# Performance work log

Measured on AMD Instinct MI355X. Metric: run time of the kernel, lower is better.

## Reference

```python
import jax, jax.numpy as jnp
import numpy as np

N, E, G = 16000, 256000, 64
H, NR, L = 128, 96, 2
CUTOFF = 6.0
EPS = 1e-10

def _ln(x, eps=1e-5):
    m = jnp.mean(x, -1, keepdims=True)
    v = jnp.mean((x - m) ** 2, -1, keepdims=True)
    return (x - m) * jax.lax.rsqrt(v + eps)

def _mlp2(x, w1, b1, w2, b2):
    return jax.nn.silu(x @ w1 + b1) @ w2 + b2

def _xav(key, shape):
    s = (2.0 / (shape[-2] + shape[-1])) ** 0.5
    return jax.random.normal(key, shape, jnp.float32) * s

def setup_inputs():
    key = jax.random.key(0)
    ks = iter(jax.random.split(key, 64))
    pos = jax.random.normal(next(ks), (N, 3), jnp.float32) * 2.0
    z = jax.random.randint(next(ks), (N,), 1, 95)
    batch = jnp.sort(jax.random.randint(next(ks), (N,), 0, G))
    src = jax.random.randint(next(ks), (E,), 0, N)
    off = jax.random.randint(next(ks), (E,), 1, N)
    dst = (src + off) % N  # no self loops -> dist > 0
    edge_index = jnp.stack([src, dst]).astype(jnp.int32)
    H3 = 3 * H
    return dict(
        pos=pos,
        z_emb_w=jax.random.normal(next(ks), (95, H), jnp.float32),
        ne_emb_w=jax.random.normal(next(ks), (95, H), jnp.float32),
        rl_w1=_xav(next(ks), (NR, H)), rl_b1=jnp.zeros((H,), jnp.float32),
        rl_w2=_xav(next(ks), (H, H)), rl_b2=jnp.zeros((H,), jnp.float32),
        sv_w=_xav(next(ks), (H, H)), sv_b=jnp.zeros((H,), jnp.float32),
        lin_w1=_xav(next(ks), (3, H // 4)), lin_b1=jnp.zeros((H // 4,), jnp.float32),
        lin_w2=_xav(next(ks), (H // 4, 1)), lin_b2=jnp.zeros((1,), jnp.float32),
        mp_ln_g=jnp.ones((L, H), jnp.float32), mp_ln_b=jnp.zeros((L, H), jnp.float32),
        mp_xw1=_xav(next(ks), (L, H, H)), mp_xb1=jnp.zeros((L, H), jnp.float32),
        mp_xw2=_xav(next(ks), (L, H, H3)), mp_xb2=jnp.zeros((L, H3), jnp.float32),
        mp_rw=_xav(next(ks), (L, NR, H3)), mp_rb=jnp.zeros((L, H3), jnp.float32),
        mp_dw1=_xav(next(ks), (L, H3 + NR, H3)), mp_db1=jnp.zeros((L, H3), jnp.float32),
        mp_dw2=_xav(next(ks), (L, H3, H3)), mp_db2=jnp.zeros((L, H3), jnp.float32),
        ft_vw=_xav(next(ks), (L, H, 2 * H)),
        ft_xw1=_xav(next(ks), (L, 2 * H, H)), ft_xb1=jnp.zeros((L, H), jnp.float32),
        ft_xw2=_xav(next(ks), (L, H, H3)), ft_xb2=jnp.zeros((L, H3), jnp.float32),
        last_w=_xav(next(ks), (H, 1)), last_b=jnp.zeros((1,), jnp.float32),
        z=z, edge_index=edge_index, batch=batch,
    )

def _forward(pos, z_emb_w, ne_emb_w, rl_w1, rl_b1, rl_w2, rl_b2, sv_w, sv_b,
             lin_w1, lin_b1, lin_w2, lin_b2, mp_ln_g, mp_ln_b, mp_xw1, mp_xb1,
             mp_xw2, mp_xb2, mp_rw, mp_rb, mp_dw1, mp_db1, mp_dw2, mp_db2,
             ft_vw, ft_xw1, ft_xb1, ft_xw2, ft_xb2, last_w, last_b,
             z, edge_index, batch):
    inv_sqrt3 = 1.0 / (3.0 ** 0.5)
    inv_sqrt_h = 1.0 / (H ** 0.5)
    inv_sqrt2 = 1.0 / (2.0 ** 0.5)
    src, dst = edge_index[0], edge_index[1]  # gather from src, scatter-add to dst
    edge_vec = pos[src] - pos[dst]                         # (E,3)
    dist = jnp.sqrt(jnp.sum(edge_vec ** 2, -1))            # (E,)
    # rbf_emb buffers
    start = jnp.exp(jnp.float32(-CUTOFF))
    means = jnp.linspace(start, 1.0, NR)
    betas = (2.0 / NR * (1.0 - start)) ** (-2.0)
    d = dist[:, None]
    rbounds = 0.5 * (jnp.cos(dist * jnp.pi / CUTOFF) + 1.0) * (dist < CUTOFF).astype(dist.dtype)
    rbf = rbounds[:, None] * jnp.exp(-betas * (jnp.exp(-d) - means) ** 2)   # (E,NR)
    rh = rbounds[:, None] * _mlp2(rbf, rl_w1, rl_b1, rl_w2, rl_b2)          # (E,H) radial_hidden
    # embeddings + NeighborEmb (gather-scale-scatter)
    s = _ln(z_emb_w[z])
    sn = _ln(ne_emb_w[z])
    s = s + jax.ops.segment_sum(rh * sn[src], dst, num_segments=N)
    vec = jnp.zeros((N, 3, H), pos.dtype)
    # edge-wise equivariant frame
    edge_diff = edge_vec / d
    edge_cross = jnp.cross(pos[src], pos[dst])
    edge_cross = edge_cross / (jnp.linalg.norm(edge_cross, axis=-1, keepdims=True) + EPS)
    edge_vertical = jnp.cross(edge_diff, edge_cross)
    edge_frame = jnp.stack([edge_diff, edge_cross, edge_vertical], -1)      # (E,3,3)
    # S_vector
    s1 = jax.nn.silu(_ln(s @ sv_w + sv_b))
    msgv = (rh[:, None, :] * edge_diff[:, :, None]) * s1[src][:, None, :]   # (E,3,H)
    S_ij = jax.ops.segment_sum(msgv, dst, num_segments=N)                   # (N,3,H)

    def _scalarize(Sg):
        sc = jnp.einsum('eck,ech->ekh', edge_frame, Sg)    # (E,3,H)
        sc = sc.at[:, 1, :].set(jnp.abs(sc[:, 1, :]))
        p = jnp.transpose(sc, (0, 2, 1))                   # (E,H,3)
        out = _mlp2(p, lin_w1, lin_b1, lin_w2, lin_b2) + p[:, :, 0:1]
        return out[..., 0]                                 # (E,H)

    scalar3 = _scalarize(S_ij[src])
    scalar4 = _scalarize(S_ij[dst])
    edge_weight = jnp.concatenate([scalar3, scalar4], -1) * rbounds[:, None]
    edge_weight = jnp.concatenate([edge_weight, rh, rbf], -1)  # (E, 3H+NR)

    for l in range(L):
        # EquiMessagePassing
        xh = _mlp2(mp_ln_g[l] * _ln(s) + mp_ln_b[l], mp_xw1[l], mp_xb1[l], mp_xw2[l], mp_xb2[l])  # (N,3H)
        rbfh = (rbf @ mp_rw[l] + mp_rb[l]) * _mlp2(edge_weight, mp_dw1[l], mp_db1[l], mp_dw2[l], mp_db2[l])
        m = xh[src] * rbfh                                  # (E,3H)
        mx, m2, m3 = jnp.split(m, 3, -1)
        m2 = m2 * inv_sqrt3
        mvec = (vec[src] * m2[:, None, :] + m3[:, None, :] * edge_diff[:, :, None]) * inv_sqrt_h
        s = (s + jax.ops.segment_sum(mx, dst, num_segments=N)) * inv_sqrt2
        vec = vec + jax.ops.segment_sum(mvec, dst, num_segments=N)
        # FTE (node_frame unused by FTE in the original code)
        vp = jnp.einsum('nch,hk->nck', vec, ft_vw[l])       # (N,3,2H)
        v1, v2 = jnp.split(vp, 2, -1)
        scalar = jnp.sqrt(jnp.sum(v1 ** 2, 1) + 1e-10)      # (N,H)
        vec_dot = jnp.sum(v1 * v2, 1) * inv_sqrt_h
        xvh = _mlp2(jnp.concatenate([s, scalar], -1), ft_xw1[l], ft_xb1[l], ft_xw2[l], ft_xb2[l])
        x1, x2, x3 = jnp.split(xvh, 3, -1)
        s = s + (x1 + x2 + vec_dot) * inv_sqrt2
        vec = vec + x3[:, None, :] * v2

    out = s @ last_w + last_b                               # (N,1)
    return jax.ops.segment_sum(out, batch, num_segments=G)  # (G,1) sum readout

def reference(pos, z_emb_w, ne_emb_w, rl_w1, rl_b1, rl_w2, rl_b2, sv_w, sv_b,
              lin_w1, lin_b1, lin_w2, lin_b2, mp_ln_g, mp_ln_b, mp_xw1, mp_xb1,
              mp_xw2, mp_xb2, mp_rw, mp_rb, mp_dw1, mp_db1, mp_dw2, mp_db2,
              ft_vw, ft_xw1, ft_xb1, ft_xw2, ft_xb2, last_w, last_b,
              z, edge_index, batch):
    return _forward(pos, z_emb_w, ne_emb_w, rl_w1, rl_b1, rl_w2, rl_b2, sv_w, sv_b,
                    lin_w1, lin_b1, lin_w2, lin_b2, mp_ln_g, mp_ln_b, mp_xw1, mp_xb1,
                    mp_xw2, mp_xb2, mp_rw, mp_rb, mp_dw1, mp_db1, mp_dw2, mp_db2,
                    ft_vw, ft_xw1, ft_xb1, ft_xw2, ft_xb2, last_w, last_b,
                    z, edge_index, batch)
```

## Files before the change

kernel.cpp:

```cpp
#include <hip/hip_runtime.h>
#include <math.h>

#define NN 16000
#define NE 256000
#define NG 64
#define HD 128
#define NRAD 96
#define H3 384
#define KD 480

typedef unsigned short u16;
typedef short short8 __attribute__((ext_vector_type(8)));
typedef float f32x4 __attribute__((ext_vector_type(4)));

__device__ __forceinline__ float siluf(float x){ return x / (1.0f + expf(-x)); }

__device__ __forceinline__ float wsum(float v){
#pragma unroll
    for (int o = 32; o > 0; o >>= 1) v += __shfl_xor(v, o, 64);
    return v;
}

__device__ __forceinline__ u16 f2bh(float f){
    unsigned int u = __float_as_uint(f);
    unsigned int r = u + 0x7FFFu + ((u >> 16) & 1u);
    return (u16)(r >> 16);
}
__device__ __forceinline__ float bh2f(u16 h){
    return __uint_as_float((unsigned int)h << 16);
}
__device__ __forceinline__ short8 ld8(const u16* p){ return *(const short8*)p; }

__device__ __forceinline__ void split4(float4 v, uint2& ph, uint2& pl){
    unsigned ux = __float_as_uint(v.x), uy = __float_as_uint(v.y);
    unsigned uz = __float_as_uint(v.z), uw = __float_as_uint(v.w);
    ph.x = __builtin_amdgcn_perm(uy, ux, 0x07060302u);
    ph.y = __builtin_amdgcn_perm(uw, uz, 0x07060302u);
    float lx = v.x - __uint_as_float(ux & 0xFFFF0000u);
    float ly = v.y - __uint_as_float(uy & 0xFFFF0000u);
    float lz = v.z - __uint_as_float(uz & 0xFFFF0000u);
    float lw = v.w - __uint_as_float(uw & 0xFFFF0000u);
    pl.x = __builtin_amdgcn_perm(__float_as_uint(ly), __float_as_uint(lx), 0x07060302u);
    pl.y = __builtin_amdgcn_perm(__float_as_uint(lw), __float_as_uint(lz), 0x07060302u);
}

__global__ void k_fill(float* __restrict__ p, float v, int n){
    int i = blockIdx.x * blockDim.x + threadIdx.x;
    if (i < n) p[i] = v;
}

__global__ void k_wsplit(const float* __restrict__ src, u16* __restrict__ dh, int K, int N){
    int i = blockIdx.x * 256 + threadIdx.x;
    if (i >= K * N) return;
    int n = i / K, k = i - n * K;
    dh[i] = f2bh(src[(size_t)k * N + n]);
}

__global__ void k_node_embed(const float* __restrict__ zw, const float* __restrict__ nw,
                             const int* __restrict__ z, float* __restrict__ s, float* __restrict__ sn){
    int n = blockIdx.x, t = threadIdx.x;
    int zi = z[n];
    const float* a = zw + (size_t)zi * HD;
    const float* b = nw + (size_t)zi * HD;
    float a0 = a[t], a1 = a[t + 64];
    float m  = wsum(a0 + a1) * (1.f / HD);
    float va = wsum((a0 - m)*(a0 - m) + (a1 - m)*(a1 - m)) * (1.f / HD);
    float r  = rsqrtf(va + 1e-5f);
    s[(size_t)n*HD + t]      = (a0 - m) * r;
    s[(size_t)n*HD + 64 + t] = (a1 - m) * r;
    float b0 = b[t], b1 = b[t + 64];
    m  = wsum(b0 + b1) * (1.f / HD);
    va = wsum((b0 - m)*(b0 - m) + (b1 - m)*(b1 - m)) * (1.f / HD);
    r  = rsqrtf(va + 1e-5f);
    sn[(size_t)n*HD + t]      = (b0 - m) * r;
    sn[(size_t)n*HD + 64 + t] = (b1 - m) * r;
}

__global__ void k_ln_silu(const float* __restrict__ x, float* __restrict__ out){
    int n = blockIdx.x, t = threadIdx.x;
    float a0 = x[(size_t)n*HD + t], a1 = x[(size_t)n*HD + 64 + t];
    float m  = wsum(a0 + a1) * (1.f / HD);
    float va = wsum((a0 - m)*(a0 - m) + (a1 - m)*(a1 - m)) * (1.f / HD);
    float r  = rsqrtf(va + 1e-5f);
    out[(size_t)n*HD + t]      = siluf((a0 - m) * r);
    out[(size_t)n*HD + 64 + t] = siluf((a1 - m) * r);
}

__global__ void k_ln_aff(const float* __restrict__ x, const float* __restrict__ g,
                         const float* __restrict__ b, float* __restrict__ out){
    int n = blockIdx.x, t = threadIdx.x;
    float a0 = x[(size_t)n*HD + t], a1 = x[(size_t)n*HD + 64 + t];
    float m  = wsum(a0 + a1) * (1.f / HD);
    float va = wsum((a0 - m)*(a0 - m) + (a1 - m)*(a1 - m)) * (1.f / HD);
    float r  = rsqrtf(va + 1e-5f);
    out[(size_t)n*HD + t]      = g[t]      * ((a0 - m) * r) + b[t];
    out[(size_t)n*HD + 64 + t] = g[64 + t] * ((a1 - m) * r) + b[64 + t];
}

__global__ void k_edge_geom(const float* __restrict__ pos, const int* __restrict__ ei,
                            float* __restrict__ dist, float* __restrict__ rbnd,
                            float* __restrict__ frame){
    int e = blockIdx.x * blockDim.x + threadIdx.x;
    if (e >= NE) return;
    int si = ei[e], di = ei[NE + e];
    float sx = pos[si*3], sy = pos[si*3+1], sz = pos[si*3+2];
    float dx = pos[di*3], dy = pos[di*3+1], dz = pos[di*3+2];
    float vx = sx - dx, vy = sy - dy, vz = sz - dz;
    float dd = sqrtf(vx*vx + vy*vy + vz*vz);
    dist[e] = dd;
    float rb = (dd < 6.0f) ? 0.5f * (cosf(dd * 0.5235987755982988f) + 1.0f) : 0.0f;
    rbnd[e] = rb;
    float inv = 1.0f / dd;
    float ux = vx*inv, uy = vy*inv, uz = vz*inv;
    float cx = sy*dz - sz*dy, cy = sz*dx - sx*dz, cz = sx*dy - sy*dx;
    float cn = sqrtf(cx*cx + cy*cy + cz*cz) + 1e-10f;
    cx /= cn; cy /= cn; cz /= cn;
    float wx = uy*cz - uz*cy, wy = uz*cx - ux*cz, wz = ux*cy - uy*cx;
    frame[(0*3+0)*NE + e] = ux; frame[(1*3+0)*NE + e] = uy; frame[(2*3+0)*NE + e] = uz;
    frame[(0*3+1)*NE + e] = cx; frame[(1*3+1)*NE + e] = cy; frame[(2*3+1)*NE + e] = cz;
    frame[(0*3+2)*NE + e] = wx; frame[(1*3+2)*NE + e] = wy; frame[(2*3+2)*NE + e] = wz;
}

__global__ void k_rbf(const float* __restrict__ dist, const float* __restrict__ rbnd,
                      float* __restrict__ base, int e0, int ec){
    int idx = blockIdx.x * 256 + threadIdx.x;
    int e = idx / NRAD;
    if (e >= ec) return;
    int k = idx - e * NRAD;
    int eg = e0 + e;
    float start = expf(-6.0f);
    float mean  = start + (1.0f - start) * ((float)k / 95.0f);
    float c     = (2.0f / 96.0f) * (1.0f - start);
    float betas = 1.0f / (c * c);
    float t = expf(-dist[eg]) - mean;
    base[(size_t)e * KD + k] = rbnd[eg] * expf(-betas * t * t);
}

__global__ __launch_bounds__(256)
void mgemm(const float* __restrict__ A, int lda,
           const u16* __restrict__ Bhg, int K,
           const float* __restrict__ bias, int act,
           float* __restrict__ C, int ldc,
           int M, int Nn,
           const float* __restrict__ row_scale,
           const float* __restrict__ mulC, int ldm){
    __shared__ u16 Ah[128*40], Al[128*40];
    __shared__ u16 Bh[64*40];
    int tid = threadIdx.x;
    int w = tid >> 6, l = tid & 63;
    int row0 = blockIdx.x * 128, col0 = blockIdx.y * 64;
    f32x4 acc[2][4] = {};
    const int r16 = l & 15, kb = (l >> 4) * 8;

    for (int k0 = 0; k0 < K; k0 += 32){
        if (k0) __syncthreads();
#pragma unroll
        for (int i = 0; i < 4; i++){
            int f = tid + i * 256;
            int r = f >> 3, kq = (f & 7) * 4;
            const float4 v = *(const float4*)(A + (size_t)(row0 + r) * lda + k0 + kq);
            uint2 ph, pl;
            split4(v, ph, pl);
            *(uint2*)&Ah[r*40 + kq] = ph;
            *(uint2*)&Al[r*40 + kq] = pl;
        }
        {
            int bn = tid >> 2, kq = (tid & 3) * 8;
            const size_t gb = (size_t)(col0 + bn) * K + k0 + kq;
            *(short8*)&Bh[bn*40 + kq] = ld8(Bhg + gb);
        }
        __syncthreads();
        short8 ah0 = *(const short8*)&Ah[(w*32      + r16)*40 + kb];
        short8 ah1 = *(const short8*)&Ah[(w*32 + 16 + r16)*40 + kb];
        short8 al0 = *(const short8*)&Al[(w*32      + r16)*40 + kb];
        short8 al1 = *(const short8*)&Al[(w*32 + 16 + r16)*40 + kb];
#pragma unroll
        for (int nf = 0; nf < 4; nf++){
            short8 bhv = *(const short8*)&Bh[(nf*16 + r16)*40 + kb];
            acc[0][nf] = __builtin_amdgcn_mfma_f32_16x16x32_bf16(ah0, bhv, acc[0][nf], 0, 0, 0);
            acc[0][nf] = __builtin_amdgcn_mfma_f32_16x16x32_bf16(al0, bhv, acc[0][nf], 0, 0, 0);
            acc[1][nf] = __builtin_amdgcn_mfma_f32_16x16x32_bf16(ah1, bhv, acc[1][nf], 0, 0, 0);
            acc[1][nf] = __builtin_amdgcn_mfma_f32_16x16x32_bf16(al1, bhv, acc[1][nf], 0, 0, 0);
        }
    }
    int rq = (l >> 4) * 4;
#pragma unroll
    for (int mf = 0; mf < 2; mf++){
#pragma unroll
        for (int nf = 0; nf < 4; nf++){
            int n = col0 + nf*16 + r16;
            float bz = bias ? bias[n] : 0.0f;
#pragma unroll
            for (int reg = 0; reg < 4; reg++){
                int m = row0 + w*32 + mf*16 + rq + reg;
                float v = acc[mf][nf][reg] + bz;
                if (act) v = siluf(v);
                if (row_scale) v *= row_scale[m];
                if (mulC) v *= mulC[(size_t)m * ldm + n];
                C[(size_t)m * ldc + n] = v;
            }
        }
    }
}

__global__ __launch_bounds__(256)
void dw2s(const float* __restrict__ hb,
          const float* __restrict__ ewrbf,
          const u16* __restrict__ B1h,
          const u16* __restrict__ B2h,
          const float* __restrict__ rb, const float* __restrict__ db2,
          const float* __restrict__ xh, const float* __restrict__ vec,
          const float* __restrict__ frame, const int* __restrict__ ei,
          float* __restrict__ s, float* __restrict__ vec_acc, int e0){
    __shared__ u16 Ah[128*40], Al[128*40];
    __shared__ u16 Bh[64*40];
    int tid = threadIdx.x;
    int w = tid >> 6, l = tid & 63;
    int row0 = blockIdx.x * 128, col0 = blockIdx.y * 64;
    const int r16 = l & 15, kb = (l >> 4) * 8;
    f32x4 acc1[2][4] = {}, acc2[2][4] = {};

    for (int k0 = 0; k0 < 96; k0 += 32){
        if (k0) __syncthreads();
#pragma unroll
        for (int i = 0; i < 4; i++){
            int f = tid + i * 256;
            int r = f >> 3, kq = (f & 7) * 4;
            const float4 v = *(const float4*)(ewrbf + (size_t)(row0 + r) * KD + k0 + kq);
            uint2 ph, pl;
            split4(v, ph, pl);
            *(uint2*)&Ah[r*40 + kq] = ph;
            *(uint2*)&Al[r*40 + kq] = pl;
        }
        {
            int bn = tid >> 2, kq = (tid & 3) * 8;
            const size_t gb = (size_t)(col0 + bn) * 96 + k0 + kq;
            *(short8*)&Bh[bn*40 + kq] = ld8(B2h + gb);
        }
        __syncthreads();
        short8 ah0 = *(const short8*)&Ah[(w*32      + r16)*40 + kb];
        short8 ah1 = *(const short8*)&Ah[(w*32 + 16 + r16)*40 + kb];
        short8 al0 = *(const short8*)&Al[(w*32      + r16)*40 + kb];
        short8 al1 = *(const short8*)&Al[(w*32 + 16 + r16)*40 + kb];
#pragma unroll
        for (int nf = 0; nf < 4; nf++){
            short8 bhv = *(const short8*)&Bh[(nf*16 + r16)*40 + kb];
            acc2[0][nf] = __builtin_amdgcn_mfma_f32_16x16x32_bf16(ah0, bhv, acc2[0][nf], 0, 0, 0);
            acc2[0][nf] = __builtin_amdgcn_mfma_f32_16x16x32_bf16(al0, bhv, acc2[0][nf], 0, 0, 0);
            acc2[1][nf] = __builtin_amdgcn_mfma_f32_16x16x32_bf16(ah1, bhv, acc2[1][nf], 0, 0, 0);
            acc2[1][nf] = __builtin_amdgcn_mfma_f32_16x16x32_bf16(al1, bhv, acc2[1][nf], 0, 0, 0);
        }
    }
    for (int k0 = 0; k0 < H3; k0 += 32){
        __syncthreads();
#pragma unroll
        for (int i = 0; i < 4; i++){
            int f = tid + i * 256;
            int r = f >> 3, kq = (f & 7) * 4;
            const float4 v = *(const float4*)(hb + (size_t)(row0 + r) * H3 + k0 + kq);
            uint2 ph, pl;
            split4(v, ph, pl);
            *(uint2*)&Ah[r*40 + kq] = ph;
            *(uint2*)&Al[r*40 + kq] = pl;
        }
        {
            int bn = tid >> 2, kq = (tid & 3) * 8;
            const size_t gb = (size_t)(col0 + bn) * H3 + k0 + kq;
            *(short8*)&Bh[bn*40 + kq] = ld8(B1h + gb);
        }
        __syncthreads();
        short8 ah0 = *(const short8*)&Ah[(w*32      + r16)*40 + kb];
        short8 ah1 = *(const short8*)&Ah[(w*32 + 16 + r16)*40 + kb];
        short8 al0 = *(const short8*)&Al[(w*32      + r16)*40 + kb];
        short8 al1 = *(const short8*)&Al[(w*32 + 16 + r16)*40 + kb];
#pragma unroll
        for (int nf = 0; nf < 4; nf++){
            short8 bhv = *(const short8*)&Bh[(nf*16 + r16)*40 + kb];
            acc1[0][nf] = __builtin_amdgcn_mfma_f32_16x16x32_bf16(ah0, bhv, acc1[0][nf], 0, 0, 0);
            acc1[0][nf] = __builtin_amdgcn_mfma_f32_16x16x32_bf16(al0, bhv, acc1[0][nf], 0, 0, 0);
            acc1[1][nf] = __builtin_amdgcn_mfma_f32_16x16x32_bf16(ah1, bhv, acc1[1][nf], 0, 0, 0);
            acc1[1][nf] = __builtin_amdgcn_mfma_f32_16x16x32_bf16(al1, bhv, acc1[1][nf], 0, 0, 0);
        }
    }
    int rq = (l >> 4) * 4;
    int br = col0 >> 7;
    int ho = col0 & 127;
#pragma unroll
    for (int mf = 0; mf < 2; mf++){
#pragma unroll
        for (int reg = 0; reg < 4; reg++){
            int m  = row0 + w*32 + mf*16 + rq + reg;
            int eg = e0 + m;
            int si = ei[eg], di = ei[NE + eg];
            float df0 = 0.f, df1 = 0.f, df2 = 0.f;
            if (br == 2){
                df0 = frame[0*NE + eg];
                df1 = frame[3*NE + eg];
                df2 = frame[6*NE + eg];
            }
#pragma unroll
            for (int nf = 0; nf < 4; nf++){
                int n = col0 + nf*16 + r16;
                int h = ho + nf*16 + r16;
                float v  = (acc2[mf][nf][reg] + rb[n]) * (acc1[mf][nf][reg] + db2[n]);
                float xv = xh[(size_t)si * H3 + n];
                if (br == 0){
                    atomicAdd(&s[(size_t)di * HD + h], xv * v);
                } else if (br == 1){
                    float m2 = xv * v * 0.5773502691896258f;
                    size_t sb = (size_t)si * H3, db = (size_t)di * H3;
#pragma unroll
                    for (int c = 0; c < 3; c++)
                        atomicAdd(&vec_acc[db + c*HD + h],
                                  vec[sb + c*HD + h] * m2 * 0.08838834764831845f);
                } else {
                    float m3 = xv * v * 0.08838834764831845f;
                    size_t db = (size_t)di * H3;
                    atomicAdd(&vec_acc[db + 0*HD + h], m3 * df0);
                    atomicAdd(&vec_acc[db + 1*HD + h], m3 * df1);
                    atomicAdd(&vec_acc[db + 2*HD + h], m3 * df2);
                }
            }
        }
    }
}

struct WT { u16* h; };

static void gemm(hipStream_t st, const float* A, int lda, WT B,
                 const float* bias, float* C, int ldc, size_t M, int K, int Nn,
                 int act, const float* rs, const float* mul, int ldm){
    dim3 g((unsigned)(M / 128), (unsigned)(Nn / 64)), b(256);
    mgemm<<<g, b, 0, st>>>(A, lda, B.h, K, bias, act, C, ldc, (int)M, Nn, rs, mul, ldm);
}

__global__ void k_scatter_s(const float* __restrict__ rh, const float* __restrict__ sn,
                            const int* __restrict__ ei, float* __restrict__ s, int e0, int ec,
                            long long stride){
    int idx = blockIdx.x * 256 + threadIdx.x;
    int e = idx >> 7, h = idx & 127;
    if (e >= ec) return;
    int eg = e0 + e;
    int si = ei[eg], di = ei[NE + eg];
    atomicAdd(&s[(size_t)di * HD + h], rh[(size_t)e * stride + h] * sn[(size_t)si * HD + h]);
}

__global__ void k_scatter_msgv(const float* __restrict__ rh, const float* __restrict__ s1,
                               const float* __restrict__ frame, const int* __restrict__ ei,
                               float* __restrict__ S_ij, int e0, int ec){
    int idx = blockIdx.x * 256 + threadIdx.x;
    int e = idx >> 7, h = idx & 127;
    if (e >= ec) return;
    int eg = e0 + e;
    int si = ei[eg], di = ei[NE + eg];
    float mv = rh[(size_t)e * KD + h] * s1[(size_t)si * HD + h];
    size_t db = (size_t)di * H3;
#pragma unroll
    for (int c = 0; c < 3; c++){
        float df = frame[(c*3 + 0) * NE + eg];
        atomicAdd(&S_ij[db + c * HD + h], mv * df);
    }
}

__global__ void k_scalarize(const float* __restrict__ S_ij, const float* __restrict__ frame,
                            const float* __restrict__ rbnd, const int* __restrict__ ei,
                            const float* __restrict__ w1, const float* __restrict__ b1,
                            const float* __restrict__ w2, const float* __restrict__ b2v,
                            float* __restrict__ base, int e0){
    int e = blockIdx.x, h = threadIdx.x;
    int eg = e0 + e;
    int si = ei[eg], di = ei[NE + eg];
    float fr[9];
#pragma unroll
    for (int i = 0; i < 9; i++) fr[i] = frame[i * NE + eg];
    float rb = rbnd[eg];
    float b2 = b2v[0];
#pragma unroll
    for (int g = 0; g < 2; g++){
        int node = g ? di : si;
        float S0 = S_ij[(size_t)node * H3 + h];
        float S1 = S_ij[(size_t)node * H3 + 128 + h];
        float S2 = S_ij[(size_t)node * H3 + 256 + h];
        float p0 = fr[0]*S0 + fr[3]*S1 + fr[6]*S2;
        float p1 = fabsf(fr[1]*S0 + fr[4]*S1 + fr[7]*S2);
        float p2 = fr[2]*S0 + fr[5]*S1 + fr[8]*S2;
        float o = b2 + p0;
#pragma unroll
        for (int j = 0; j < 32; j++){
            float hh = siluf(p0 * w1[j] + p1 * w1[32 + j] + p2 * w1[64 + j] + b1[j]);
            o += hh * w2[j];
        }
        base[(size_t)e * KD + g * 128 + h] = o * rb;
    }
}

__global__ void k_scale_vecadd(float* __restrict__ s, float* __restrict__ vec,
                               const float* __restrict__ vec_acc){
    int i = blockIdx.x * 256 + threadIdx.x;
    vec[i] += vec_acc[i];
    int n = i / H3, r = i - n * H3;
    if (r < HD) s[(size_t)n * HD + r] *= 0.7071067811865476f;
}

__global__ void k_vfeat(const float* __restrict__ vp, const float* __restrict__ s,
                        float* __restrict__ t256, float* __restrict__ vdot){
    int idx = blockIdx.x * 256 + threadIdx.x;
    int n = idx >> 7, h = idx & 127;
    float a = 0.f, b = 0.f;
#pragma unroll
    for (int c = 0; c < 3; c++){
        float v1 = vp[(size_t)(n*3 + c) * 256 + h];
        float v2 = vp[(size_t)(n*3 + c) * 256 + 128 + h];
        a += v1 * v1;
        b += v1 * v2;
    }
    t256[(size_t)n * 256 + 128 + h] = sqrtf(a + 1e-10f);
    vdot[idx] = b * 0.08838834764831845f;
    t256[(size_t)n * 256 + h] = s[idx];
}

__global__ void k_upd(float* __restrict__ s, float* __restrict__ vec,
                      const float* __restrict__ xvh, const float* __restrict__ vp,
                      const float* __restrict__ vdot){
    int idx = blockIdx.x * 256 + threadIdx.x;
    int n = idx / H3;
    int r = idx - n * H3;
    int c = r >> 7, h = r & 127;
    vec[idx] += xvh[(size_t)n * H3 + 256 + h] * vp[(size_t)(n*3 + c) * 256 + 128 + h];
    if (c == 0){
        size_t si = (size_t)n * HD + h;
        s[si] += (xvh[(size_t)n * H3 + h] + xvh[(size_t)n * H3 + 128 + h]
                  + vdot[si]) * 0.7071067811865476f;
    }
}

__global__ void k_final(const float* __restrict__ s, const float* __restrict__ lw,
                        const float* __restrict__ lb, const int* __restrict__ batch,
                        float* __restrict__ out){
    int n = blockIdx.x, t = threadIdx.x;
    float v = s[(size_t)n * HD + t] * lw[t] + s[(size_t)n * HD + 64 + t] * lw[64 + t];
    v = wsum(v);
    if (t == 0) atomicAdd(&out[batch[n]], v + lb[0]);
}

extern "C" void kernel_launch(void* const* d_in, const int* in_sizes, int n_in,
                              void* d_out, int out_size, void* d_ws, size_t ws_size,
                              hipStream_t stream){
    const float* pos      = (const float*)d_in[0];
    const float* z_emb_w  = (const float*)d_in[1];
    const float* ne_emb_w = (const float*)d_in[2];
    const float* rl_w1    = (const float*)d_in[3];
    const float* rl_b1    = (const float*)d_in[4];
    const float* rl_w2    = (const float*)d_in[5];
    const float* rl_b2    = (const float*)d_in[6];
    const float* sv_w     = (const float*)d_in[7];
    const float* sv_b     = (const float*)d_in[8];
    const float* lin_w1   = (const float*)d_in[9];
    const float* lin_b1   = (const float*)d_in[10];
    const float* lin_w2   = (const float*)d_in[11];
    const float* lin_b2   = (const float*)d_in[12];
    const float* mp_ln_g  = (const float*)d_in[13];
    const float* mp_ln_b  = (const float*)d_in[14];
    const float* mp_xw1   = (const float*)d_in[15];
    const float* mp_xb1   = (const float*)d_in[16];
    const float* mp_xw2   = (const float*)d_in[17];
    const float* mp_xb2   = (const float*)d_in[18];
    const float* mp_rw    = (const float*)d_in[19];
    const float* mp_rb    = (const float*)d_in[20];
    const float* mp_dw1   = (const float*)d_in[21];
    const float* mp_db1   = (const float*)d_in[22];
    const float* mp_dw2   = (const float*)d_in[23];
    const float* mp_db2   = (const float*)d_in[24];
    const float* ft_vw    = (const float*)d_in[25];
    const float* ft_xw1   = (const float*)d_in[26];
    const float* ft_xb1   = (const float*)d_in[27];
    const float* ft_xw2   = (const float*)d_in[28];
    const float* ft_xb2   = (const float*)d_in[29];
    const float* last_w   = (const float*)d_in[30];
    const float* last_b   = (const float*)d_in[31];
    const int*   z        = (const int*)d_in[32];
    const int*   ei       = (const int*)d_in[33];
    const int*   batch    = (const int*)d_in[34];
    float* out = (float*)d_out;
    (void)in_sizes; (void)n_in; (void)out_size;

    float* ws = (float*)d_ws;
    size_t off = 0;
    auto alloc = [&](size_t nf){ float* p = ws + off; off += (nf + 63) & ~(size_t)63; return p; };

    float* s       = alloc((size_t)NN * HD);
    float* sn      = alloc((size_t)NN * HD);
    float* s1      = alloc((size_t)NN * HD);
    float* tA      = alloc((size_t)NN * HD);
    float* vdot    = alloc((size_t)NN * HD);
    float* vec     = alloc((size_t)NN * H3);
    float* vec_acc = alloc((size_t)NN * H3);
    float* S_ij    = alloc((size_t)NN * H3);
    float* xh      = alloc((size_t)NN * H3);
    float* vp      = alloc((size_t)NN * 3 * 256);
    float* dist    = alloc((size_t)NE);
    float* rbnd    = alloc((size_t)NE);
    float* frame   = alloc((size_t)NE * 9);
    float* t256    = sn;

    const size_t WELEMS = 45056 + 2 * 548864;
    u16* wcur = (u16*)alloc((WELEMS + 1) / 2);
    auto wsplit = [&](const float* src, int K, int N)->WT{
        WT r; r.h = wcur; wcur += (size_t)K * N;
        k_wsplit<<<(unsigned)(((size_t)K * N + 255) / 256), 256, 0, stream>>>(src, r.h, K, N);
        return r;
    };
    WT W_rl1 = wsplit(rl_w1, NRAD, HD);
    WT W_rl2 = wsplit(rl_w2, HD, HD);
    WT W_sv  = wsplit(sv_w, HD, HD);
    WT W_xw1[2], W_xw2[2], W_rw[2], W_dw1[2], W_dw2[2], W_vw[2], W_fx1[2], W_fx2[2];
    for (int l = 0; l < 2; l++){
        W_xw1[l] = wsplit(mp_xw1 + (size_t)l * HD * HD, HD, HD);
        W_xw2[l] = wsplit(mp_xw2 + (size_t)l * HD * H3, HD, H3);
        W_rw[l]  = wsplit(mp_rw  + (size_t)l * NRAD * H3, NRAD, H3);
        W_dw1[l] = wsplit(mp_dw1 + (size_t)l * KD * H3, KD, H3);
        W_dw2[l] = wsplit(mp_dw2 + (size_t)l * H3 * H3, H3, H3);
        W_vw[l]  = wsplit(ft_vw  + (size_t)l * HD * 256, HD, 256);
        W_fx1[l] = wsplit(ft_xw1 + (size_t)l * 256 * HD, 256, HD);
        W_fx2[l] = wsplit(ft_xw2 + (size_t)l * HD * H3, HD, H3);
    }

    size_t availF = ws_size / sizeof(float);
    size_t rem = (availF > off + 1024) ? (availF - off - 1024) : 0;
    const size_t EWF = (size_t)NE * KD;
    bool persist;
    size_t CE;
    float* ew  = nullptr;
    float* ewc = nullptr;
    if (rem >= EWF + 128 * 384 + 256){
        persist = true;
        ew = alloc(EWF);
        rem = availF - off - 1024;
        size_t ce = rem / (size_t)H3;
        CE = ce & ~(size_t)127;
        if (CE < 128) CE = 128;
        if (CE > NE) CE = NE;
    } else {
        persist = false;
        size_t ce = rem / ((size_t)KD + (size_t)H3);
        CE = ce & ~(size_t)127;
        if (CE < 128) CE = 128;
        if (CE > NE) CE = NE;
    }
    if (CE > 32768) CE = 32768;
    if (!persist) ewc = alloc(CE * KD);
    size_t hbufF = CE * (size_t)H3;
    bool full_layer = false;
    if (persist){
        size_t remNow = (availF > off + 1024) ? (availF - off - 1024) : 0;
        const size_t FULLH = (size_t)NE * H3;
        if (remNow >= FULLH){ hbufF = FULLH; full_layer = true; }
    }
    float* hbuf = alloc(hbufF);

    auto build_rh = [&](size_t e0, size_t ec, float* base){
        k_rbf<<<(unsigned)((ec * NRAD) / 256), 256, 0, stream>>>(dist, rbnd, base + 384, (int)e0, (int)ec);
        gemm(stream, base + 384, KD, W_rl1, rl_b1, hbuf, HD, ec, NRAD, HD, 1, nullptr, nullptr, 0);
        gemm(stream, hbuf, HD, W_rl2, rl_b2, base + 256, KD, ec, HD, HD, 0, rbnd + e0, nullptr, 0);
    };

    k_fill<<<1, 64, 0, stream>>>(out, 0.f, NG);
    k_node_embed<<<NN, 64, 0, stream>>>(z_emb_w, ne_emb_w, z, s, sn);
    k_edge_geom<<<NE / 256, 256, 0, stream>>>(pos, ei, dist, rbnd, frame);

    if (persist){
        k_rbf<<<(unsigned)(((size_t)NE * NRAD) / 256), 256, 0, stream>>>(dist, rbnd, ew + 384, 0, NE);
        if (full_layer){
            gemm(stream, ew + 384, KD, W_rl1, rl_b1, hbuf, HD, NE, NRAD, HD, 1, nullptr, nullptr, 0);
            gemm(stream, hbuf, HD, W_rl2, rl_b2, ew + 256, KD, NE, HD, HD, 0, rbnd, nullptr, 0);
        } else {
            for (size_t e0 = 0; e0 < NE; e0 += CE){
                size_t ec = (NE - e0 < CE) ? (NE - e0) : CE;
                float* base = ew + e0 * KD;
                gemm(stream, base + 384, KD, W_rl1, rl_b1, hbuf, HD, ec, NRAD, HD, 1, nullptr, nullptr, 0);
                gemm(stream, hbuf, HD, W_rl2, rl_b2, base + 256, KD, ec, HD, HD, 0, rbnd + e0, nullptr, 0);
            }
        }
        k_scatter_s<<<(unsigned)(((size_t)NE * HD) / 256), 256, 0, stream>>>(ew + 256, sn, ei, s, 0, NE, KD);
    } else {
        for (size_t e0 = 0; e0 < NE; e0 += CE){
            size_t ec = (NE - e0 < CE) ? (NE - e0) : CE;
            build_rh(e0, ec, ewc);
            k_scatter_s<<<(unsigned)((ec * HD) / 256), 256, 0, stream>>>(ewc + 256, sn, ei, s, (int)e0, (int)ec, KD);
        }
    }

    gemm(stream, s, HD, W_sv, sv_b, tA, HD, NN, HD, HD, 0, nullptr, nullptr, 0);
    k_ln_silu<<<NN, 64, 0, stream>>>(tA, s1);

    k_fill<<<(NN * H3) / 256, 256, 0, stream>>>(S_ij, 0.f, NN * H3);
    if (persist){
        k_scatter_msgv<<<(unsigned)(((size_t)NE * HD) / 256), 256, 0, stream>>>(ew + 256, s1, frame, ei, S_ij, 0, NE);
        k_scalarize<<<NE, 128, 0, stream>>>(S_ij, frame, rbnd, ei, lin_w1, lin_b1, lin_w2, lin_b2, ew, 0);
    } else {
        for (size_t e0 = 0; e0 < NE; e0 += CE){
            size_t ec = (NE - e0 < CE) ? (NE - e0) : CE;
            build_rh(e0, ec, ewc);
            k_scatter_msgv<<<(unsigned)((ec * HD) / 256), 256, 0, stream>>>(ewc + 256, s1, frame, ei, S_ij, (int)e0, (int)ec);
        }
    }

    k_fill<<<(NN * H3) / 256, 256, 0, stream>>>(vec, 0.f, NN * H3);

    for (int l = 0; l < 2; l++){
        k_ln_aff<<<NN, 64, 0, stream>>>(s, mp_ln_g + l * HD, mp_ln_b + l * HD, tA);
        gemm(stream, tA, HD, W_xw1[l], mp_xb1 + l * HD, vdot, HD, NN, HD, HD, 1, nullptr, nullptr, 0);
        gemm(stream, vdot, HD, W_xw2[l], mp_xb2 + l * H3, xh, H3, NN, HD, H3, 0, nullptr, nullptr, 0);

        k_fill<<<(NN * H3) / 256, 256, 0, stream>>>(vec_acc, 0.f, NN * H3);

        if (full_layer){
            gemm(stream, ew, KD, W_dw1[l], mp_db1 + l * H3, hbuf, H3, NE, KD, H3, 1, nullptr, nullptr, 0);
            dim3 g((unsigned)(NE / 128), 6);
            dw2s<<<g, 256, 0, stream>>>(hbuf, ew + 384,
                                        W_dw2[l].h, W_rw[l].h,
                                        mp_rb + l * H3, mp_db2 + l * H3,
                                        xh, vec, frame, ei, s, vec_acc, 0);
        } else {
            for (size_t e0 = 0; e0 < NE; e0 += CE){
                size_t ec = (NE - e0 < CE) ? (NE - e0) : CE;
                float* base = persist ? (ew + e0 * KD) : ewc;
                if (!persist){
                    build_rh(e0, ec, base);
                    k_scalarize<<<(unsigned)ec, 128, 0, stream>>>(S_ij, frame, rbnd, ei, lin_w1, lin_b1, lin_w2, lin_b2, base, (int)e0);
                }
                gemm(stream, base, KD, W_dw1[l], mp_db1 + l * H3, hbuf, H3, ec, KD, H3, 1, nullptr, nullptr, 0);
                dim3 g((unsigned)(ec / 128), 6);
                dw2s<<<g, 256, 0, stream>>>(hbuf, base + 384,
                                            W_dw2[l].h, W_rw[l].h,
                                            mp_rb + l * H3, mp_db2 + l * H3,
                                            xh, vec, frame, ei, s, vec_acc, (int)e0);
            }
        }
        k_scale_vecadd<<<(NN * H3) / 256, 256, 0, stream>>>(s, vec, vec_acc);

        gemm(stream, vec, HD, W_vw[l], nullptr, vp, 256, (size_t)NN * 3, HD, 256, 0, nullptr, nullptr, 0);
        k_vfeat<<<(NN * HD) / 256, 256, 0, stream>>>(vp, s, t256, vdot);

        gemm(stream, t256, 256, W_fx1[l], ft_xb1 + l * HD, tA, HD, NN, 256, HD, 1, nullptr, nullptr, 0);
        gemm(stream, tA, HD, W_fx2[l], ft_xb2 + l * H3, xh, H3, NN, HD, H3, 0, nullptr, nullptr, 0);

        k_upd<<<(NN * H3) / 256, 256, 0, stream>>>(s, vec, xh, vp, vdot);
    }

    k_final<<<NN, 64, 0, stream>>>(s, last_w, last_b, batch, out);
}
```

Measured before the change: 10.06 ms.

## Store hidden edge activations as bf16 and drop low-part MFMA in dw2s

Adds a GEMM variant that writes the dw1 hidden activations (NE x 384) directly as bf16 instead of fp32. The dw2s kernel now loads them as bf16 and skips the hi/lo split, halving its MFMAs on the main K loop. The hidden buffer also shrinks by half, and the rl-MLP scratch gets its own buffer. This cuts memory traffic and compute on the largest per-edge GEMM chain. In exchange it loses precision on that intermediate, since it was previously carried as split bf16 (effectively near-fp32).

```diff
diff --git a/kernel.cpp b/kernel.cpp
--- a/kernel.cpp
+++ b/kernel.cpp
@@ -204,7 +204,70 @@
 }
 
 __global__ __launch_bounds__(256)
-void dw2s(const float* __restrict__ hb,
+void mgemmb(const float* __restrict__ A, int lda,
+            const u16* __restrict__ Bhg, int K,
+            const float* __restrict__ bias, int act,
+            u16* __restrict__ C, int ldc,
+            int M, int Nn){
+    __shared__ u16 Ah[128*40], Al[128*40];
+    __shared__ u16 Bh[64*40];
+    int tid = threadIdx.x;
+    int w = tid >> 6, l = tid & 63;
+    int row0 = blockIdx.x * 128, col0 = blockIdx.y * 64;
+    f32x4 acc[2][4] = {};
+    const int r16 = l & 15, kb = (l >> 4) * 8;
+
+    for (int k0 = 0; k0 < K; k0 += 32){
+        if (k0) __syncthreads();
+#pragma unroll
+        for (int i = 0; i < 4; i++){
+            int f = tid + i * 256;
+            int r = f >> 3, kq = (f & 7) * 4;
+            const float4 v = *(const float4*)(A + (size_t)(row0 + r) * lda + k0 + kq);
+            uint2 ph, pl;
+            split4(v, ph, pl);
+            *(uint2*)&Ah[r*40 + kq] = ph;
+            *(uint2*)&Al[r*40 + kq] = pl;
+        }
+        {
+            int bn = tid >> 2, kq = (tid & 3) * 8;
+            const size_t gb = (size_t)(col0 + bn) * K + k0 + kq;
+            *(short8*)&Bh[bn*40 + kq] = ld8(Bhg + gb);
+        }
+        __syncthreads();
+        short8 ah0 = *(const short8*)&Ah[(w*32      + r16)*40 + kb];
+        short8 ah1 = *(const short8*)&Ah[(w*32 + 16 + r16)*40 + kb];
+        short8 al0 = *(const short8*)&Al[(w*32      + r16)*40 + kb];
+        short8 al1 = *(const short8*)&Al[(w*32 + 16 + r16)*40 + kb];
+#pragma unroll
+        for (int nf = 0; nf < 4; nf++){
+            short8 bhv = *(const short8*)&Bh[(nf*16 + r16)*40 + kb];
+            acc[0][nf] = __builtin_amdgcn_mfma_f32_16x16x32_bf16(ah0, bhv, acc[0][nf], 0, 0, 0);
+            acc[0][nf] = __builtin_amdgcn_mfma_f32_16x16x32_bf16(al0, bhv, acc[0][nf], 0, 0, 0);
+            acc[1][nf] = __builtin_amdgcn_mfma_f32_16x16x32_bf16(ah1, bhv, acc[1][nf], 0, 0, 0);
+            acc[1][nf] = __builtin_amdgcn_mfma_f32_16x16x32_bf16(al1, bhv, acc[1][nf], 0, 0, 0);
+        }
+    }
+    int rq = (l >> 4) * 4;
+#pragma unroll
+    for (int mf = 0; mf < 2; mf++){
+#pragma unroll
+        for (int nf = 0; nf < 4; nf++){
+            int n = col0 + nf*16 + r16;
+            float bz = bias ? bias[n] : 0.0f;
+#pragma unroll
+            for (int reg = 0; reg < 4; reg++){
+                int m = row0 + w*32 + mf*16 + rq + reg;
+                float v = acc[mf][nf][reg] + bz;
+                if (act) v = siluf(v);
+                C[(size_t)m * ldc + n] = f2bh(v);
+            }
+        }
+    }
+}
+
+__global__ __launch_bounds__(256)
+void dw2s(const u16* __restrict__ hb,
           const float* __restrict__ ewrbf,
           const u16* __restrict__ B1h,
           const u16* __restrict__ B2h,
@@ -253,15 +316,11 @@
     }
     for (int k0 = 0; k0 < H3; k0 += 32){
         __syncthreads();
-#pragma unroll
-        for (int i = 0; i < 4; i++){
-            int f = tid + i * 256;
-            int r = f >> 3, kq = (f & 7) * 4;
-            const float4 v = *(const float4*)(hb + (size_t)(row0 + r) * H3 + k0 + kq);
-            uint2 ph, pl;
-            split4(v, ph, pl);
-            *(uint2*)&Ah[r*40 + kq] = ph;
-            *(uint2*)&Al[r*40 + kq] = pl;
+        {
+            int r = tid >> 1, kq = (tid & 1) * 16;
+            const size_t gb = (size_t)(row0 + r) * H3 + k0 + kq;
+            *(short8*)&Ah[r*40 + kq]     = ld8(hb + gb);
+            *(short8*)&Ah[r*40 + kq + 8] = ld8(hb + gb + 8);
         }
         {
             int bn = tid >> 2, kq = (tid & 3) * 8;
@@ -271,15 +330,11 @@
         __syncthreads();
         short8 ah0 = *(const short8*)&Ah[(w*32      + r16)*40 + kb];
         short8 ah1 = *(const short8*)&Ah[(w*32 + 16 + r16)*40 + kb];
-        short8 al0 = *(const short8*)&Al[(w*32      + r16)*40 + kb];
-        short8 al1 = *(const short8*)&Al[(w*32 + 16 + r16)*40 + kb];
 #pragma unroll
         for (int nf = 0; nf < 4; nf++){
             short8 bhv = *(const short8*)&Bh[(nf*16 + r16)*40 + kb];
             acc1[0][nf] = __builtin_amdgcn_mfma_f32_16x16x32_bf16(ah0, bhv, acc1[0][nf], 0, 0, 0);
-            acc1[0][nf] = __builtin_amdgcn_mfma_f32_16x16x32_bf16(al0, bhv, acc1[0][nf], 0, 0, 0);
             acc1[1][nf] = __builtin_amdgcn_mfma_f32_16x16x32_bf16(ah1, bhv, acc1[1][nf], 0, 0, 0);
-            acc1[1][nf] = __builtin_amdgcn_mfma_f32_16x16x32_bf16(al1, bhv, acc1[1][nf], 0, 0, 0);
         }
     }
     int rq = (l >> 4) * 4;
@@ -332,6 +387,12 @@
                  int act, const float* rs, const float* mul, int ldm){
     dim3 g((unsigned)(M / 128), (unsigned)(Nn / 64)), b(256);
     mgemm<<<g, b, 0, st>>>(A, lda, B.h, K, bias, act, C, ldc, (int)M, Nn, rs, mul, ldm);
+}
+
+static void gemmb(hipStream_t st, const float* A, int lda, WT B,
+                  const float* bias, u16* C, int ldc, size_t M, int K, int Nn, int act){
+    dim3 g((unsigned)(M / 128), (unsigned)(Nn / 64)), b(256);
+    mgemmb<<<g, b, 0, st>>>(A, lda, B.h, K, bias, act, C, ldc, (int)M, Nn);
 }
 
 __global__ void k_scatter_s(const float* __restrict__ rh, const float* __restrict__ sn,
@@ -549,19 +610,27 @@
     }
     if (CE > 32768) CE = 32768;
     if (!persist) ewc = alloc(CE * KD);
-    size_t hbufF = CE * (size_t)H3;
+
+    size_t remNow = (availF > off + 1024) ? (availF - off - 1024) : 0;
     bool full_layer = false;
     if (persist){
-        size_t remNow = (availF > off + 1024) ? (availF - off - 1024) : 0;
-        const size_t FULLH = (size_t)NE * H3;
-        if (remNow >= FULLH){ hbufF = FULLH; full_layer = true; }
-    }
-    float* hbuf = alloc(hbufF);
+        const size_t NEED = (size_t)NE * HD + (size_t)NE * (H3 / 2);
+        if (remNow >= NEED) full_layer = true;
+    }
+    float* rlh;
+    u16*   hbuf;
+    if (full_layer){
+        rlh  = alloc((size_t)NE * HD);
+        hbuf = (u16*)alloc((size_t)NE * (H3 / 2));
+    } else {
+        rlh  = alloc((size_t)CE * HD);
+        hbuf = (u16*)alloc((size_t)CE * (H3 / 2));
+    }
 
     auto build_rh = [&](size_t e0, size_t ec, float* base){
         k_rbf<<<(unsigned)((ec * NRAD) / 256), 256, 0, stream>>>(dist, rbnd, base + 384, (int)e0, (int)ec);
-        gemm(stream, base + 384, KD, W_rl1, rl_b1, hbuf, HD, ec, NRAD, HD, 1, nullptr, nullptr, 0);
-        gemm(stream, hbuf, HD, W_rl2, rl_b2, base + 256, KD, ec, HD, HD, 0, rbnd + e0, nullptr, 0);
+        gemm(stream, base + 384, KD, W_rl1, rl_b1, rlh, HD, ec, NRAD, HD, 1, nullptr, nullptr, 0);
+        gemm(stream, rlh, HD, W_rl2, rl_b2, base + 256, KD, ec, HD, HD, 0, rbnd + e0, nullptr, 0);
     };
 
     k_fill<<<1, 64, 0, stream>>>(out, 0.f, NG);
@@ -571,14 +640,14 @@
     if (persist){
         k_rbf<<<(unsigned)(((size_t)NE * NRAD) / 256), 256, 0, stream>>>(dist, rbnd, ew + 384, 0, NE);
         if (full_layer){
-            gemm(stream, ew + 384, KD, W_rl1, rl_b1, hbuf, HD, NE, NRAD, HD, 1, nullptr, nullptr, 0);
-            gemm(stream, hbuf, HD, W_rl2, rl_b2, ew + 256, KD, NE, HD, HD, 0, rbnd, nullptr, 0);
+            gemm(stream, ew + 384, KD, W_rl1, rl_b1, rlh, HD, NE, NRAD, HD, 1, nullptr, nullptr, 0);
+            gemm(stream, rlh, HD, W_rl2, rl_b2, ew + 256, KD, NE, HD, HD, 0, rbnd, nullptr, 0);
         } else {
             for (size_t e0 = 0; e0 < NE; e0 += CE){
                 size_t ec = (NE - e0 < CE) ? (NE - e0) : CE;
                 float* base = ew + e0 * KD;
-                gemm(stream, base + 384, KD, W_rl1, rl_b1, hbuf, HD, ec, NRAD, HD, 1, nullptr, nullptr, 0);
-                gemm(stream, hbuf, HD, W_rl2, rl_b2, base + 256, KD, ec, HD, HD, 0, rbnd + e0, nullptr, 0);
+                gemm(stream, base + 384, KD, W_rl1, rl_b1, rlh, HD, ec, NRAD, HD, 1, nullptr, nullptr, 0);
+                gemm(stream, rlh, HD, W_rl2, rl_b2, base + 256, KD, ec, HD, HD, 0, rbnd + e0, nullptr, 0);
             }
         }
         k_scatter_s<<<(unsigned)(((size_t)NE * HD) / 256), 256, 0, stream>>>(ew + 256, sn, ei, s, 0, NE, KD);
@@ -615,7 +684,7 @@
         k_fill<<<(NN * H3) / 256, 256, 0, stream>>>(vec_acc, 0.f, NN * H3);
 
         if (full_layer){
-            gemm(stream, ew, KD, W_dw1[l], mp_db1 + l * H3, hbuf, H3, NE, KD, H3, 1, nullptr, nullptr, 0);
+            gemmb(stream, ew, KD, W_dw1[l], mp_db1 + l * H3, hbuf, H3, NE, KD, H3, 1);
             dim3 g((unsigned)(NE / 128), 6);
             dw2s<<<g, 256, 0, stream>>>(hbuf, ew + 384,
                                         W_dw2[l].h, W_rw[l].h,
@@ -629,7 +698,7 @@
                     build_rh(e0, ec, base);
                     k_scalarize<<<(unsigned)ec, 128, 0, stream>>>(S_ij, frame, rbnd, ei, lin_w1, lin_b1, lin_w2, lin_b2, base, (int)e0);
                 }
-                gemm(stream, base, KD, W_dw1[l], mp_db1 + l * H3, hbuf, H3, ec, KD, H3, 1, nullptr, nullptr, 0);
+                gemmb(stream, base, KD, W_dw1[l], mp_db1 + l * H3, hbuf, H3, ec, KD, H3, 1);
                 dim3 g((unsigned)(ec / 128), 6);
                 dw2s<<<g, 256, 0, stream>>>(hbuf, base + 384,
                                             W_dw2[l].h, W_rw[l].h,
```

Result: no change. 10.12 ms (+0.6%).
